# Performance work log

Hardware: AMD Instinct MI355X
Metric: run time of the kernel (lower is better)

Reference implementation:

```python
import jax, jax.numpy as jnp
import numpy as np

L, B, T, TC, T1, D, DK, FF = 4, 4, 1024, 1024, 2048, 384, 256, 1536
TT = 0.1   # lamed blending coefficient (tt in (0,1] path)
EPS = 1e-5


def _ln(x, g, b):
    m = jnp.mean(x, axis=-1, keepdims=True)
    v = jnp.mean((x - m) ** 2, axis=-1, keepdims=True)
    return (x - m) * jax.lax.rsqrt(v + EPS) * g + b


def setup_inputs() -> dict:
    key = jax.random.key(0)
    ks = jax.random.split(key, 16)
    s = 0.02
    return {
        "tgt": jax.random.normal(ks[0], (B, T, D), jnp.float32),
        "memory": jax.random.normal(ks[1], (B, T1, DK), jnp.float32),
        "score_c": jax.random.normal(ks[2], (L, B, TC, T1), jnp.float32),
        "out_c": jax.random.normal(ks[3], (L, B, TC, D), jnp.float32),
        "Wq": jax.random.normal(ks[4], (L, D, D), jnp.float32) * s,
        "bq": jnp.zeros((L, D), jnp.float32),
        "Wk": jax.random.normal(ks[5], (L, D, DK), jnp.float32) * s,
        "bk": jnp.zeros((L, D), jnp.float32),
        "Wv": jax.random.normal(ks[6], (L, D, DK), jnp.float32) * s,
        "bv": jnp.zeros((L, D), jnp.float32),
        "Wkn": jax.random.normal(ks[7], (L, D, D), jnp.float32) * s,
        "bkn": jnp.zeros((L, D), jnp.float32),
        "Wun": jax.random.normal(ks[8], (L, D, D), jnp.float32) * s,
        "bun": jnp.zeros((L, D), jnp.float32),
        "W1": jax.random.normal(ks[9], (L, FF, D), jnp.float32) * s,
        "b1": jnp.zeros((L, FF), jnp.float32),
        "W2": jax.random.normal(ks[10], (L, D, FF), jnp.float32) * s,
        "b2": jnp.zeros((L, D), jnp.float32),
        "g1": jnp.ones((L, D), jnp.float32),
        "be1": jnp.zeros((L, D), jnp.float32),
        "g2": jnp.ones((L, D), jnp.float32),
        "be2": jnp.zeros((L, D), jnp.float32),
    }


def reference(tgt, memory, score_c, out_c, Wq, bq, Wk, bk, Wv, bv,
              Wkn, bkn, Wun, bun, W1, b1, W2, b2, g1, be1, g2, be2):
    scale = 1.0 / np.sqrt(D)
    x = tgt
    for l in range(L):  # fixed small layer count
        # cross-attention q/k/v (n_head = 1)
        q = jnp.einsum('btd,ed->bte', x, Wq[l]) + bq[l]            # [B,T,D]
        k = jnp.einsum('bsk,ek->bse', memory, Wk[l]) + bk[l]       # [B,T1,D]
        v = jnp.einsum('bsk,ek->bse', memory, Wv[l]) + bv[l]       # [B,T1,D]
        att = jnp.einsum('bte,bse->bts', q, k) * scale             # [B,T,T1]
        # blended score path (tt in (0,1])
        unk = jnp.einsum('btd,ed->bte', x, Wun[l]) + bun[l]        # [B,T,D]
        kno = jnp.einsum('bcd,ed->bce', out_c[l], Wkn[l]) + bkn[l] # [B,TC,D]
        score1 = jnp.einsum('bte,bce->btc', unk, kno) * scale      # [B,T,TC]
        mixed = jnp.einsum('btc,bcs->bts', score1, score_c[l])     # [B,T,T1]
        blended = TT * jax.nn.softmax(mixed, axis=-1) \
                  + (1.0 - TT) * jax.nn.softmax(att, axis=-1)
        z = jnp.einsum('bts,bse->bte', blended, v)                 # [B,T,D]
        x = _ln(x + z, g1[l], be1[l])
        h = jax.nn.relu(jnp.einsum('btd,fd->btf', x, W1[l]) + b1[l])
        y2 = jnp.einsum('btf,df->btd', h, W2[l]) + b2[l]
        x = _ln(x + y2, g2[l], be2[l])
    return x
```

## Files before the change

kernel.cpp:

```cpp
#include <hip/hip_runtime.h>
#include <math.h>

#define Lc 4
#define Bc 4
#define Tc 1024
#define TCc 1024
#define T1c 2048
#define Dc 384
#define DKc 256
#define FFc 1536
#define TTc 0.1f
#define EPSc 1e-5f
#define QUc 640

typedef unsigned short u16;
typedef __attribute__((ext_vector_type(8))) __bf16 bf16x8;
typedef __attribute__((ext_vector_type(8))) _Float16 f16x8;
typedef __attribute__((ext_vector_type(4))) float f32x4;

__device__ inline u16 f2bf(float f) {
  union { float f; unsigned u; } x; x.f = f;
  unsigned r = x.u + 0x7fffu + ((x.u >> 16) & 1u);
  return (u16)(r >> 16);
}
__device__ inline float bf2f(u16 v) {
  union { unsigned u; float f; } x; x.u = (unsigned)v << 16; return x.f;
}

struct CDesc { const float* src; u16* dst; long n4; };
struct CPack { CDesc d[16]; long tot4; int nd; };

__global__ void cvt_multi(CPack P) {
  long i = (long)blockIdx.x * 256 + threadIdx.x;
  const long st = (long)gridDim.x * 256;
  for (; i < P.tot4; i += st) {
    long r = i; int g = 0;
    while (g < P.nd - 1 && r >= P.d[g].n4) { r -= P.d[g].n4; ++g; }
    float4 v = ((const float4*)P.d[g].src)[r];
    ushort4 o;
    o.x = f2bf(v.x); o.y = f2bf(v.y); o.z = f2bf(v.z); o.w = f2bf(v.w);
    ((ushort4*)P.d[g].dst)[r] = o;
  }
}

__global__ void make_bias(const float* __restrict__ bq, const float* __restrict__ bun,
                          const u16* __restrict__ wkT, float* __restrict__ bqu) {
  const int l = blockIdx.x, t = threadIdx.x;
  if (t < DKc) {
    const u16* w = wkT + ((long)l * DKc + t) * Dc;
    const float* b = bq + l * Dc;
    float s = 0.f;
    for (int e = 0; e < Dc; ++e) s += b[e] * bf2f(w[e]);
    bqu[l * QUc + t] = s;
  } else {
    bqu[l * QUc + t] = bun[l * Dc + (t - DKc)];
  }
}

__global__ __launch_bounds__(256) void transpose_cvt(const float* __restrict__ src,
                                                     u16* __restrict__ dst,
                                                     int R, int C) {
  __shared__ float t[64 * 65];
  const int z = blockIdx.z;
  const float* s = src + (long)z * R * C;
  u16* d = dst + (long)z * R * C;
  const int s0 = blockIdx.x * 64, c0 = blockIdx.y * 64;
  const int tc = threadIdx.x >> 4;
  const int tx = (threadIdx.x & 15) * 4;
#pragma unroll
  for (int it = 0; it < 4; ++it) {
    const int c = tc + it * 16;
    float4 v = *(const float4*)(s + (long)(c0 + c) * C + s0 + tx);
    float* q = t + c * 65 + tx;
    q[0] = v.x; q[1] = v.y; q[2] = v.z; q[3] = v.w;
  }
  __syncthreads();
#pragma unroll
  for (int it = 0; it < 4; ++it) {
    const int srow = tc + it * 16;
    u16 o[4];
#pragma unroll
    for (int k2 = 0; k2 < 4; ++k2) o[k2] = f2bf(t[(tx + k2) * 65 + srow]);
    *(ushort4*)(d + (long)(s0 + srow) * R + c0 + tx) = *(ushort4*)o;
  }
}

template<int BIAS_MODE, int RELU, int OUT_MODE, int SWIZ, int DUAL>
__global__ __launch_bounds__(256) void gemm_bt(
    const u16* __restrict__ A, const u16* __restrict__ B,
    void* __restrict__ C, const float* __restrict__ bias,
    float alpha, int N, int K, int lda, int ldb,
    long sA, long sB, long sC, long sBias, int ksplit, long sSlab, int bdivA,
    const u16* __restrict__ B2, int ldb2, long sB2, int aoff2,
    void* __restrict__ C2, float alpha2, int nbat, int K2)
{
  __shared__ __attribute__((aligned(16))) u16 As[2][128 * 32];
  __shared__ __attribute__((aligned(16))) u16 Bs[2][128 * 32];
  const int bz = blockIdx.z;
  int b = bz / ksplit;
  const int kc = bz - b * ksplit;
  const u16* Bp = B; int ldbv = ldb; long sBv = sB; void* Cp = C;
  int aoff = 0; float al = alpha; int Kv = K;
  if (DUAL && b >= nbat) {
    b -= nbat; Bp = B2; ldbv = ldb2; sBv = sB2; Cp = C2;
    aoff = aoff2; al = alpha2; Kv = K2;
  }
  const int ba = b / bdivA;
  const int Klen = Kv / ksplit;
  const int k0 = kc * Klen;
  const u16* Ab = A + (long)ba * sA + aoff;
  const u16* Bb = Bp + (long)b * sBv;
  long tm, tn;
  if (SWIZ) {
    const int id = blockIdx.y * 16 + blockIdx.x;
    tm = (long)(id >> 4) * 128;
    tn = (long)(2 * (id & 7) + ((id >> 3) & 1)) * 128;
  } else {
    tm = (long)blockIdx.y * 128; tn = (long)blockIdx.x * 128;
  }
  const int tid = threadIdx.x;
  const int lane = tid & 63, wv = tid >> 6;
  const int wm = (wv >> 1) * 64, wn = (wv & 1) * 64;
  const int q = lane >> 4, r = lane & 15;
  const int ldr = lane >> 2;
  const int ldc = (lane & 3) * 8;

  const u16* gA0 = Ab + (tm + wv * 32 + ldr) * (long)lda + k0 + ldc;
  const u16* gA1 = gA0 + 16 * (long)lda;
  const u16* gB0 = Bb + (tn + wv * 32 + ldr) * (long)ldbv + k0 + ldc;
  const u16* gB1 = gB0 + 16 * (long)ldbv;
  const int dof = (wv * 32 + ldr) * 32 + ldc;

  const f32x4 zero4 = {0.0f, 0.0f, 0.0f, 0.0f};
  f32x4 acc[4][4];
#pragma unroll
  for (int i = 0; i < 4; ++i)
#pragma unroll
    for (int j = 0; j < 4; ++j) acc[i][j] = zero4;

  uint4 ra0 = *(const uint4*)gA0;
  uint4 ra1 = *(const uint4*)gA1;
  uint4 rb0 = *(const uint4*)gB0;
  uint4 rb1 = *(const uint4*)gB1;

  const int iters = Klen >> 5;
  int cur = 0;
  for (int it = 0; it < iters; ++it) {
    u16* a0 = As[cur] + dof;
    u16* b0 = Bs[cur] + dof;
    *(uint4*)a0 = ra0; *(uint4*)(a0 + 512) = ra1;
    *(uint4*)b0 = rb0; *(uint4*)(b0 + 512) = rb1;
    if (it + 1 < iters) {
      const long o = (long)(it + 1) * 32;
      ra0 = *(const uint4*)(gA0 + o);
      ra1 = *(const uint4*)(gA1 + o);
      rb0 = *(const uint4*)(gB0 + o);
      rb1 = *(const uint4*)(gB1 + o);
    }
    __syncthreads();
    bf16x8 af[4], bfr[4];
#pragma unroll
    for (int i = 0; i < 4; ++i) {
      af[i]  = *(const bf16x8*)(As[cur] + (wm + i * 16 + r) * 32 + q * 8);
      bfr[i] = *(const bf16x8*)(Bs[cur] + (wn + i * 16 + r) * 32 + q * 8);
    }
#pragma unroll
    for (int i = 0; i < 4; ++i)
#pragma unroll
      for (int j = 0; j < 4; ++j)
        acc[i][j] = __builtin_amdgcn_mfma_f32_16x16x32_bf16(af[i], bfr[j], acc[i][j], 0, 0, 0);
    cur ^= 1;
  }

  const float* biasb = bias ? bias + (long)ba * sBias : nullptr;
#pragma unroll
  for (int i = 0; i < 4; ++i)
#pragma unroll
    for (int j = 0; j < 4; ++j)
#pragma unroll
      for (int v = 0; v < 4; ++v) {
        long row = tm + wm + i * 16 + q * 4 + v;
        long col = tn + wn + j * 16 + r;
        float val = acc[i][j][v] * al;
        if (BIAS_MODE == 1 && kc == 0) val += biasb[col];
        if (BIAS_MODE == 2 && kc == 0) val += biasb[row];
        if (RELU) val = fmaxf(val, 0.0f);
        long idx = (long)kc * sSlab + (long)b * sC + row * (long)N + col;
        if (OUT_MODE == 0)      ((float*)Cp)[idx] = val;
        else if (OUT_MODE == 1) ((u16*)Cp)[idx] = f2bf(val);
        else                    ((_Float16*)Cp)[idx] = (_Float16)val;
      }
}

__global__ __launch_bounds__(256) void blend_softmax(
    const _Float16* __restrict__ att, const _Float16* __restrict__ mixed,
    u16* __restrict__ out)
{
  const long row = blockIdx.x;
  const int tid = threadIdx.x;
  f16x8 av = *(const f16x8*)(att + row * T1c + tid * 8);
  f16x8 mv = *(const f16x8*)(mixed + row * T1c + tid * 8);
  float a[8], m[8];
#pragma unroll
  for (int i = 0; i < 8; ++i) { a[i] = (float)av[i]; m[i] = (float)mv[i]; }
  float amax = a[0], mmax = m[0];
#pragma unroll
  for (int i = 1; i < 8; ++i) { amax = fmaxf(amax, a[i]); mmax = fmaxf(mmax, m[i]); }
#pragma unroll
  for (int off = 32; off > 0; off >>= 1) {
    amax = fmaxf(amax, __shfl_xor(amax, off));
    mmax = fmaxf(mmax, __shfl_xor(mmax, off));
  }
  __shared__ float red[8];
  const int lane = tid & 63, wv = tid >> 6;
  if (lane == 0) { red[wv] = amax; red[4 + wv] = mmax; }
  __syncthreads();
  amax = fmaxf(fmaxf(red[0], red[1]), fmaxf(red[2], red[3]));
  mmax = fmaxf(fmaxf(red[4], red[5]), fmaxf(red[6], red[7]));
  __syncthreads();
  float asum = 0.f, msum = 0.f;
#pragma unroll
  for (int i = 0; i < 8; ++i) {
    a[i] = __expf(a[i] - amax); asum += a[i];
    m[i] = __expf(m[i] - mmax); msum += m[i];
  }
#pragma unroll
  for (int off = 32; off > 0; off >>= 1) {
    asum += __shfl_xor(asum, off);
    msum += __shfl_xor(msum, off);
  }
  if (lane == 0) { red[wv] = asum; red[4 + wv] = msum; }
  __syncthreads();
  asum = red[0] + red[1] + red[2] + red[3];
  msum = red[4] + red[5] + red[6] + red[7];
  const float ca = (1.0f - TTc) / asum, cm = TTc / msum;
  u16 o[8];
#pragma unroll
  for (int i = 0; i < 8; ++i) o[i] = f2bf(a[i] * ca + m[i] * cm);
  *(uint4*)(out + row * T1c + tid * 8) = *(uint4*)o;
}

__global__ __launch_bounds__(384) void add_ln4(
    const float* __restrict__ xin, const float* __restrict__ zs,
    const float* __restrict__ g, const float* __restrict__ be,
    float* __restrict__ xout, u16* __restrict__ xbf)
{
  const long row = blockIdx.x;
  const int d = threadIdx.x;
  const long SL = (long)Bc * Tc * Dc;
  const long o = row * Dc + d;
  float v = xin[o] + zs[o] + zs[SL + o] + zs[2 * SL + o] + zs[3 * SL + o];
  float s = v, s2 = v * v;
#pragma unroll
  for (int off = 32; off > 0; off >>= 1) {
    s  += __shfl_xor(s, off);
    s2 += __shfl_xor(s2, off);
  }
  __shared__ float red[12];
  const int lane = d & 63, wv = d >> 6;
  if (lane == 0) { red[wv] = s; red[6 + wv] = s2; }
  __syncthreads();
  float S = 0.f, S2 = 0.f;
#pragma unroll
  for (int w = 0; w < 6; ++w) { S += red[w]; S2 += red[6 + w]; }
  const float mean = S * (1.0f / Dc);
  const float var  = S2 * (1.0f / Dc) - mean * mean;
  const float rstd = rsqrtf(var + EPSc);
  const float y = (v - mean) * rstd * g[d] + be[d];
  xout[o] = y;
  xbf[o] = f2bf(y);
}

extern "C" void kernel_launch(void* const* d_in, const int* in_sizes, int n_in,
                              void* d_out, int out_size, void* d_ws, size_t ws_size,
                              hipStream_t stream)
{
  const float* tgt     = (const float*)d_in[0];
  const float* memory  = (const float*)d_in[1];
  const float* score_c = (const float*)d_in[2];
  const float* out_c   = (const float*)d_in[3];
  const float* Wq  = (const float*)d_in[4];  const float* bq  = (const float*)d_in[5];
  const float* Wk  = (const float*)d_in[6];  const float* bk  = (const float*)d_in[7];
  const float* Wv  = (const float*)d_in[8];  const float* bv  = (const float*)d_in[9];
  const float* Wkn = (const float*)d_in[10]; const float* bkn = (const float*)d_in[11];
  const float* Wun = (const float*)d_in[12]; const float* bun = (const float*)d_in[13];
  const float* W1  = (const float*)d_in[14]; const float* b1  = (const float*)d_in[15];
  const float* W2  = (const float*)d_in[16]; const float* b2  = (const float*)d_in[17];
  const float* g1  = (const float*)d_in[18]; const float* be1 = (const float*)d_in[19];
  const float* g2  = (const float*)d_in[20]; const float* be2 = (const float*)d_in[21];
  (void)bk; (void)in_sizes; (void)n_in; (void)out_size;

  char* p = (char*)d_ws;
  auto alloc = [&](size_t b) { char* r = p; p += (b + 255) & ~(size_t)255; return r; };

  u16* wv_bf   = (u16*)alloc((size_t)Lc * Dc * DKc * 2);
  u16* wkn_bf  = (u16*)alloc((size_t)Lc * Dc * Dc * 2);
  u16* w1_bf   = (u16*)alloc((size_t)Lc * FFc * Dc * 2);
  u16* w2_bf   = (u16*)alloc((size_t)Lc * Dc * FFc * 2);
  u16* wqT     = (u16*)alloc((size_t)Lc * Dc * Dc * 2);
  u16* wkT     = (u16*)alloc((size_t)Lc * DKc * Dc * 2);
  u16* wqu_bf  = (u16*)alloc((size_t)Lc * QUc * Dc * 2);
  float* bqu   = (float*)alloc((size_t)Lc * QUc * 4);
  u16* mem_bf  = (u16*)alloc((size_t)Bc * T1c * DKc * 2);
  u16* outc_bf = (u16*)alloc((size_t)Lc * Bc * TCc * Dc * 2);
  u16* x_bf    = (u16*)alloc((size_t)Bc * Tc * Dc * 2);
  float* xbuf  = (float*)alloc((size_t)Bc * Tc * Dc * 4);
  u16* qunk_bf = (u16*)alloc((size_t)Bc * Tc * QUc * 2);
  u16* vT_all  = (u16*)alloc((size_t)Bc * Lc * Dc * T1c * 2);
  u16* knoT_all = (u16*)alloc((size_t)Lc * Bc * Dc * TCc * 2);
  u16* M2T_all = (u16*)alloc((size_t)Lc * Bc * T1c * Dc * 2);
  u16* scT_all = (u16*)alloc((size_t)Lc * Bc * T1c * TCc * 2);
  _Float16* att   = (_Float16*)alloc((size_t)Bc * Tc * T1c * 2);
  _Float16* mixed = (_Float16*)alloc((size_t)Bc * Tc * T1c * 2);
  u16* blended = (u16*)alloc((size_t)Bc * Tc * T1c * 2);
  float* zslab = (float*)alloc((size_t)4 * Bc * Tc * Dc * 4);
  float* yslab = (float*)alloc((size_t)4 * Bc * Tc * Dc * 4);
  u16* h_bf    = (u16*)alloc((size_t)Bc * Tc * FFc * 2);

  if ((size_t)(p - (char*)d_ws) > ws_size) return;

  {
    CPack cp{}; int g = 0; long tot4 = 0;
    auto add = [&](const float* s, u16* d, long n) {
      cp.d[g].src = s; cp.d[g].dst = d; cp.d[g].n4 = n / 4; tot4 += n / 4; ++g;
    };
    add(Wv,  wv_bf,  (long)Lc * Dc * DKc);
    add(Wkn, wkn_bf, (long)Lc * Dc * Dc);
    add(W1,  w1_bf,  (long)Lc * FFc * Dc);
    add(W2,  w2_bf,  (long)Lc * Dc * FFc);
    add(memory, mem_bf, (long)Bc * T1c * DKc);
    add(out_c, outc_bf, (long)Lc * Bc * TCc * Dc);
    add(tgt, x_bf, (long)Bc * Tc * Dc);
    for (int l = 0; l < Lc; ++l)
      add(Wun + (long)l * Dc * Dc,
          wqu_bf + (long)l * QUc * Dc + (long)DKc * Dc, (long)Dc * Dc);
    cp.nd = g; cp.tot4 = tot4;
    cvt_multi<<<4096, 256, 0, stream>>>(cp);
  }

  transpose_cvt<<<dim3(T1c / 64, TCc / 64, Lc * Bc), 256, 0, stream>>>(
      score_c, scT_all, TCc, T1c);
  transpose_cvt<<<dim3(Dc / 64, Dc / 64, Lc), 256, 0, stream>>>(Wq, wqT, Dc, Dc);
  transpose_cvt<<<dim3(DKc / 64, Dc / 64, Lc), 256, 0, stream>>>(Wk, wkT, Dc, DKc);

  const float scale = 1.0f / sqrtf((float)Dc);
  const long SLAB = (long)Bc * Tc * Dc;

  gemm_bt<0,0,1,0,0><<<dim3(Dc/128, DKc/128, Lc), 256, 0, stream>>>(
      wkT, wqT, wqu_bf, nullptr, 1.0f, Dc, Dc, Dc, Dc,
      (long)DKc*Dc, (long)Dc*Dc, (long)QUc*Dc, 0, 1, 0, 1,
      nullptr, 0, 0, 0, nullptr, 0.f, 0, Dc);
  make_bias<<<Lc, QUc, 0, stream>>>(bq, bun, wkT, bqu);

  gemm_bt<2,0,1,0,0><<<dim3(T1c/128, Lc*Dc/128, Bc), 256, 0, stream>>>(
      wv_bf, mem_bf, vT_all, bv, 1.0f, T1c, DKc, DKc, DKc,
      0, (long)T1c*DKc, (long)Lc*Dc*T1c, 0, 1, 0, 1,
      nullptr, 0, 0, 0, nullptr, 0.f, 0, DKc);
  gemm_bt<2,0,1,0,0><<<dim3(TCc/128, Dc/128, Lc*Bc), 256, 0, stream>>>(
      wkn_bf, outc_bf, knoT_all, bkn, 1.0f, TCc, Dc, Dc, Dc,
      (long)Dc*Dc, (long)TCc*Dc, (long)Dc*TCc, Dc, 1, 0, Bc,
      nullptr, 0, 0, 0, nullptr, 0.f, 0, Dc);
  gemm_bt<0,0,1,0,0><<<dim3(Dc/128, T1c/128, Lc*Bc), 256, 0, stream>>>(
      scT_all, knoT_all, M2T_all, nullptr, scale, Dc, TCc, TCc, TCc,
      (long)T1c*TCc, (long)Dc*TCc, (long)T1c*Dc, 0, 1, 0, 1,
      nullptr, 0, 0, 0, nullptr, 0.f, 0, TCc);

  for (int l = 0; l < Lc; ++l) {
    gemm_bt<1,0,1,0,0><<<dim3(QUc/128, Bc*Tc/128, 1), 256, 0, stream>>>(
        x_bf, wqu_bf + (long)l*QUc*Dc, qunk_bf, bqu + l*QUc,
        1.0f, QUc, Dc, Dc, Dc, 0, 0, 0, 0, 1, 0, 1,
        nullptr, 0, 0, 0, nullptr, 0.f, 0, Dc);
    gemm_bt<0,0,2,1,1><<<dim3(T1c/128, Tc/128, 2*Bc), 256, 0, stream>>>(
        qunk_bf, mem_bf, att, nullptr, scale, T1c, DKc, QUc, DKc,
        (long)Tc*QUc, (long)T1c*DKc, (long)Tc*T1c, 0, 1, 0, 1,
        M2T_all + (long)l*Bc*T1c*Dc, Dc, (long)T1c*Dc, DKc, mixed, 1.0f, Bc, Dc);
    blend_softmax<<<Bc*Tc, 256, 0, stream>>>(att, mixed, blended);
    gemm_bt<0,0,0,0,0><<<dim3(Dc/128, Tc/128, Bc*4), 256, 0, stream>>>(
        blended, vT_all + (long)l*Dc*T1c, zslab, nullptr, 1.0f,
        Dc, T1c, T1c, T1c, (long)Tc*T1c, (long)Lc*Dc*T1c, (long)Tc*Dc, 0, 4, SLAB, 1,
        nullptr, 0, 0, 0, nullptr, 0.f, 0, T1c);
    add_ln4<<<Bc*Tc, Dc, 0, stream>>>(
        (l == 0) ? tgt : xbuf, zslab, g1 + l*Dc, be1 + l*Dc, xbuf, x_bf);
    gemm_bt<1,1,1,0,0><<<dim3(FFc/128, Bc*Tc/128, 1), 256, 0, stream>>>(
        x_bf, w1_bf + (long)l*FFc*Dc, h_bf, b1 + l*FFc, 1.0f,
        FFc, Dc, Dc, Dc, 0, 0, 0, 0, 1, 0, 1,
        nullptr, 0, 0, 0, nullptr, 0.f, 0, Dc);
    gemm_bt<1,0,0,0,0><<<dim3(Dc/128, Bc*Tc/128, 4), 256, 0, stream>>>(
        h_bf, w2_bf + (long)l*Dc*FFc, yslab, b2 + l*Dc, 1.0f,
        Dc, FFc, FFc, FFc, 0, 0, 0, 0, 4, SLAB, 1,
        nullptr, 0, 0, 0, nullptr, 0.f, 0, FFc);
    add_ln4<<<Bc*Tc, Dc, 0, stream>>>(
        xbuf, yslab, g2 + l*Dc, be2 + l*Dc,
        (l == Lc - 1) ? (float*)d_out : xbuf, x_bf);
  }
}
```

Before: 939.2 us.

## Fuse blended softmax into attention-V GEMM A-load and read out_c as fp32

Replaces the blend_softmax kernel with a per-row stats kernel that writes only max and scale for both softmaxes. The z GEMM's A-operand load then reads the fp16 att and mixed tiles and rebuilds the blended bf16 probabilities on the fly. This removes the write and reread of the blended matrix. Separately, the kno GEMM now reads out_c directly as fp32 and converts it to bf16 while staging into shared memory, dropping that slice of the conversion pass. The cost is that every N-tile of the z GEMM reads twice the A data and recomputes the exponentials redundantly.

```diff
diff --git a/kernel.cpp b/kernel.cpp
--- a/kernel.cpp
+++ b/kernel.cpp
@@ -85,14 +85,15 @@
   }
 }
 
-template<int BIAS_MODE, int RELU, int OUT_MODE, int SWIZ, int DUAL>
+template<int BIAS_MODE, int RELU, int OUT_MODE, int SWIZ, int DUAL, int FUSEA, int BF32>
 __global__ __launch_bounds__(256) void gemm_bt(
     const u16* __restrict__ A, const u16* __restrict__ B,
     void* __restrict__ C, const float* __restrict__ bias,
     float alpha, int N, int K, int lda, int ldb,
     long sA, long sB, long sC, long sBias, int ksplit, long sSlab, int bdivA,
     const u16* __restrict__ B2, int ldb2, long sB2, int aoff2,
-    void* __restrict__ C2, float alpha2, int nbat, int K2)
+    void* __restrict__ C2, float alpha2, int nbat, int K2,
+    const u16* __restrict__ Am, const float* __restrict__ st4)
 {
   __shared__ __attribute__((aligned(16))) u16 As[2][128 * 32];
   __shared__ __attribute__((aligned(16))) u16 Bs[2][128 * 32];
@@ -138,24 +139,78 @@
 #pragma unroll
     for (int j = 0; j < 4; ++j) acc[i][j] = zero4;
 
-  uint4 ra0 = *(const uint4*)gA0;
-  uint4 ra1 = *(const uint4*)gA1;
-  uint4 rb0 = *(const uint4*)gB0;
-  uint4 rb1 = *(const uint4*)gB1;
+  uint4 ra0, ra1, rb0, rb1;
+  f16x8 av0, av1, mv0, mv1;
+  float4 qb0a, qb0b, qb1a, qb1b;
+  const u16* gM0 = nullptr; const u16* gM1 = nullptr;
+  const float* fB0 = nullptr; const float* fB1 = nullptr;
+  float4 st0, st1;
+  if (FUSEA) {
+    gM0 = Am + (gA0 - A);
+    gM1 = Am + (gA1 - A);
+    av0 = *(const f16x8*)gA0; mv0 = *(const f16x8*)gM0;
+    av1 = *(const f16x8*)gA1; mv1 = *(const f16x8*)gM1;
+    const long r0 = (long)b * Tc + tm + wv * 32 + ldr;
+    st0 = ((const float4*)st4)[r0];
+    st1 = ((const float4*)st4)[r0 + 16];
+  } else {
+    ra0 = *(const uint4*)gA0; ra1 = *(const uint4*)gA1;
+  }
+  if (BF32) {
+    const float* Bf = (const float*)B + (long)b * sBv;
+    fB0 = Bf + (tn + wv * 32 + ldr) * (long)ldbv + k0 + ldc;
+    fB1 = fB0 + 16 * (long)ldbv;
+    qb0a = *(const float4*)fB0; qb0b = *(const float4*)(fB0 + 4);
+    qb1a = *(const float4*)fB1; qb1b = *(const float4*)(fB1 + 4);
+  } else {
+    rb0 = *(const uint4*)gB0; rb1 = *(const uint4*)gB1;
+  }
 
   const int iters = Klen >> 5;
   int cur = 0;
   for (int it = 0; it < iters; ++it) {
     u16* a0 = As[cur] + dof;
     u16* b0 = Bs[cur] + dof;
-    *(uint4*)a0 = ra0; *(uint4*)(a0 + 512) = ra1;
-    *(uint4*)b0 = rb0; *(uint4*)(b0 + 512) = rb1;
+    if (FUSEA) {
+      u16 oa[16];
+#pragma unroll
+      for (int e2 = 0; e2 < 8; ++e2) {
+        oa[e2]     = f2bf(__expf((float)av0[e2] - st0.x) * st0.y
+                        + __expf((float)mv0[e2] - st0.z) * st0.w);
+        oa[8 + e2] = f2bf(__expf((float)av1[e2] - st1.x) * st1.y
+                        + __expf((float)mv1[e2] - st1.z) * st1.w);
+      }
+      *(uint4*)a0 = ((uint4*)oa)[0]; *(uint4*)(a0 + 512) = ((uint4*)oa)[1];
+    } else {
+      *(uint4*)a0 = ra0; *(uint4*)(a0 + 512) = ra1;
+    }
+    if (BF32) {
+      u16 ob[16];
+#pragma unroll
+      for (int e2 = 0; e2 < 4; ++e2) {
+        ob[e2]      = f2bf(((const float*)&qb0a)[e2]);
+        ob[4 + e2]  = f2bf(((const float*)&qb0b)[e2]);
+        ob[8 + e2]  = f2bf(((const float*)&qb1a)[e2]);
+        ob[12 + e2] = f2bf(((const float*)&qb1b)[e2]);
+      }
+      *(uint4*)b0 = ((uint4*)ob)[0]; *(uint4*)(b0 + 512) = ((uint4*)ob)[1];
+    } else {
+      *(uint4*)b0 = rb0; *(uint4*)(b0 + 512) = rb1;
+    }
     if (it + 1 < iters) {
       const long o = (long)(it + 1) * 32;
-      ra0 = *(const uint4*)(gA0 + o);
-      ra1 = *(const uint4*)(gA1 + o);
-      rb0 = *(const uint4*)(gB0 + o);
-      rb1 = *(const uint4*)(gB1 + o);
+      if (FUSEA) {
+        av0 = *(const f16x8*)(gA0 + o); mv0 = *(const f16x8*)(gM0 + o);
+        av1 = *(const f16x8*)(gA1 + o); mv1 = *(const f16x8*)(gM1 + o);
+      } else {
+        ra0 = *(const uint4*)(gA0 + o); ra1 = *(const uint4*)(gA1 + o);
+      }
+      if (BF32) {
+        qb0a = *(const float4*)(fB0 + o); qb0b = *(const float4*)(fB0 + o + 4);
+        qb1a = *(const float4*)(fB1 + o); qb1b = *(const float4*)(fB1 + o + 4);
+      } else {
+        rb0 = *(const uint4*)(gB0 + o); rb1 = *(const uint4*)(gB1 + o);
+      }
     }
     __syncthreads();
     bf16x8 af[4], bfr[4];
@@ -192,9 +247,9 @@
       }
 }
 
-__global__ __launch_bounds__(256) void blend_softmax(
+__global__ __launch_bounds__(256) void blend_stats(
     const _Float16* __restrict__ att, const _Float16* __restrict__ mixed,
-    u16* __restrict__ out)
+    float4* __restrict__ st)
 {
   const long row = blockIdx.x;
   const int tid = threadIdx.x;
@@ -221,8 +276,8 @@
   float asum = 0.f, msum = 0.f;
 #pragma unroll
   for (int i = 0; i < 8; ++i) {
-    a[i] = __expf(a[i] - amax); asum += a[i];
-    m[i] = __expf(m[i] - mmax); msum += m[i];
+    asum += __expf(a[i] - amax);
+    msum += __expf(m[i] - mmax);
   }
 #pragma unroll
   for (int off = 32; off > 0; off >>= 1) {
@@ -233,11 +288,12 @@
   __syncthreads();
   asum = red[0] + red[1] + red[2] + red[3];
   msum = red[4] + red[5] + red[6] + red[7];
-  const float ca = (1.0f - TTc) / asum, cm = TTc / msum;
-  u16 o[8];
-#pragma unroll
-  for (int i = 0; i < 8; ++i) o[i] = f2bf(a[i] * ca + m[i] * cm);
-  *(uint4*)(out + row * T1c + tid * 8) = *(uint4*)o;
+  if (tid == 0) {
+    float4 o;
+    o.x = amax; o.y = (1.0f - TTc) / asum;
+    o.z = mmax; o.w = TTc / msum;
+    st[row] = o;
+  }
 }
 
 __global__ __launch_bounds__(384) void add_ln4(
@@ -302,7 +358,6 @@
   u16* wqu_bf  = (u16*)alloc((size_t)Lc * QUc * Dc * 2);
   float* bqu   = (float*)alloc((size_t)Lc * QUc * 4);
   u16* mem_bf  = (u16*)alloc((size_t)Bc * T1c * DKc * 2);
-  u16* outc_bf = (u16*)alloc((size_t)Lc * Bc * TCc * Dc * 2);
   u16* x_bf    = (u16*)alloc((size_t)Bc * Tc * Dc * 2);
   float* xbuf  = (float*)alloc((size_t)Bc * Tc * Dc * 4);
   u16* qunk_bf = (u16*)alloc((size_t)Bc * Tc * QUc * 2);
@@ -312,7 +367,7 @@
   u16* scT_all = (u16*)alloc((size_t)Lc * Bc * T1c * TCc * 2);
   _Float16* att   = (_Float16*)alloc((size_t)Bc * Tc * T1c * 2);
   _Float16* mixed = (_Float16*)alloc((size_t)Bc * Tc * T1c * 2);
-  u16* blended = (u16*)alloc((size_t)Bc * Tc * T1c * 2);
+  float4* stats = (float4*)alloc((size_t)Bc * Tc * 16);
   float* zslab = (float*)alloc((size_t)4 * Bc * Tc * Dc * 4);
   float* yslab = (float*)alloc((size_t)4 * Bc * Tc * Dc * 4);
   u16* h_bf    = (u16*)alloc((size_t)Bc * Tc * FFc * 2);
@@ -329,7 +384,6 @@
     add(W1,  w1_bf,  (long)Lc * FFc * Dc);
     add(W2,  w2_bf,  (long)Lc * Dc * FFc);
     add(memory, mem_bf, (long)Bc * T1c * DKc);
-    add(out_c, outc_bf, (long)Lc * Bc * TCc * Dc);
     add(tgt, x_bf, (long)Bc * Tc * Dc);
     for (int l = 0; l < Lc; ++l)
       add(Wun + (long)l * Dc * Dc,
@@ -346,49 +400,51 @@
   const float scale = 1.0f / sqrtf((float)Dc);
   const long SLAB = (long)Bc * Tc * Dc;
 
-  gemm_bt<0,0,1,0,0><<<dim3(Dc/128, DKc/128, Lc), 256, 0, stream>>>(
+  gemm_bt<0,0,1,0,0,0,0><<<dim3(Dc/128, DKc/128, Lc), 256, 0, stream>>>(
       wkT, wqT, wqu_bf, nullptr, 1.0f, Dc, Dc, Dc, Dc,
       (long)DKc*Dc, (long)Dc*Dc, (long)QUc*Dc, 0, 1, 0, 1,
-      nullptr, 0, 0, 0, nullptr, 0.f, 0, Dc);
+      nullptr, 0, 0, 0, nullptr, 0.f, 0, Dc, nullptr, nullptr);
   make_bias<<<Lc, QUc, 0, stream>>>(bq, bun, wkT, bqu);
 
-  gemm_bt<2,0,1,0,0><<<dim3(T1c/128, Lc*Dc/128, Bc), 256, 0, stream>>>(
+  gemm_bt<2,0,1,0,0,0,0><<<dim3(T1c/128, Lc*Dc/128, Bc), 256, 0, stream>>>(
       wv_bf, mem_bf, vT_all, bv, 1.0f, T1c, DKc, DKc, DKc,
       0, (long)T1c*DKc, (long)Lc*Dc*T1c, 0, 1, 0, 1,
-      nullptr, 0, 0, 0, nullptr, 0.f, 0, DKc);
-  gemm_bt<2,0,1,0,0><<<dim3(TCc/128, Dc/128, Lc*Bc), 256, 0, stream>>>(
-      wkn_bf, outc_bf, knoT_all, bkn, 1.0f, TCc, Dc, Dc, Dc,
+      nullptr, 0, 0, 0, nullptr, 0.f, 0, DKc, nullptr, nullptr);
+  gemm_bt<2,0,1,0,0,0,1><<<dim3(TCc/128, Dc/128, Lc*Bc), 256, 0, stream>>>(
+      wkn_bf, (const u16*)out_c, knoT_all, bkn, 1.0f, TCc, Dc, Dc, Dc,
       (long)Dc*Dc, (long)TCc*Dc, (long)Dc*TCc, Dc, 1, 0, Bc,
-      nullptr, 0, 0, 0, nullptr, 0.f, 0, Dc);
-  gemm_bt<0,0,1,0,0><<<dim3(Dc/128, T1c/128, Lc*Bc), 256, 0, stream>>>(
+      nullptr, 0, 0, 0, nullptr, 0.f, 0, Dc, nullptr, nullptr);
+  gemm_bt<0,0,1,0,0,0,0><<<dim3(Dc/128, T1c/128, Lc*Bc), 256, 0, stream>>>(
       scT_all, knoT_all, M2T_all, nullptr, scale, Dc, TCc, TCc, TCc,
       (long)T1c*TCc, (long)Dc*TCc, (long)T1c*Dc, 0, 1, 0, 1,
-      nullptr, 0, 0, 0, nullptr, 0.f, 0, TCc);
+      nullptr, 0, 0, 0, nullptr, 0.f, 0, TCc, nullptr, nullptr);
 
   for (int l = 0; l < Lc; ++l) {
-    gemm_bt<1,0,1,0,0><<<dim3(QUc/128, Bc*Tc/128, 1), 256, 0, stream>>>(
+    gemm_bt<1,0,1,0,0,0,0><<<dim3(QUc/128, Bc*Tc/128, 1), 256, 0, stream>>>(
         x_bf, wqu_bf + (long)l*QUc*Dc, qunk_bf, bqu + l*QUc,
         1.0f, QUc, Dc, Dc, Dc, 0, 0, 0, 0, 1, 0, 1,
-        nullptr, 0, 0, 0, nullptr, 0.f, 0, Dc);
-    gemm_bt<0,0,2,1,1><<<dim3(T1c/128, Tc/128, 2*Bc), 256, 0, stream>>>(
+        nullptr, 0, 0, 0, nullptr, 0.f, 0, Dc, nullptr, nullptr);
+    gemm_bt<0,0,2,1,1,0,0><<<dim3(T1c/128, Tc/128, 2*Bc), 256, 0, stream>>>(
         qunk_bf, mem_bf, att, nullptr, scale, T1c, DKc, QUc, DKc,
         (long)Tc*QUc, (long)T1c*DKc, (long)Tc*T1c, 0, 1, 0, 1,
-        M2T_all + (long)l*Bc*T1c*Dc, Dc, (long)T1c*Dc, DKc, mixed, 1.0f, Bc, Dc);
-    blend_softmax<<<Bc*Tc, 256, 0, stream>>>(att, mixed, blended);
-    gemm_bt<0,0,0,0,0><<<dim3(Dc/128, Tc/128, Bc*4), 256, 0, stream>>>(
-        blended, vT_all + (long)l*Dc*T1c, zslab, nullptr, 1.0f,
+        M2T_all + (long)l*Bc*T1c*Dc, Dc, (long)T1c*Dc, DKc, mixed, 1.0f, Bc, Dc,
+        nullptr, nullptr);
+    blend_stats<<<Bc*Tc, 256, 0, stream>>>(att, mixed, stats);
+    gemm_bt<0,0,0,0,0,1,0><<<dim3(Dc/128, Tc/128, Bc*4), 256, 0, stream>>>(
+        (const u16*)att, vT_all + (long)l*Dc*T1c, zslab, nullptr, 1.0f,
         Dc, T1c, T1c, T1c, (long)Tc*T1c, (long)Lc*Dc*T1c, (long)Tc*Dc, 0, 4, SLAB, 1,
-        nullptr, 0, 0, 0, nullptr, 0.f, 0, T1c);
+        nullptr, 0, 0, 0, nullptr, 0.f, 0, T1c,
+        (const u16*)mixed, (const float*)stats);
     add_ln4<<<Bc*Tc, Dc, 0, stream>>>(
         (l == 0) ? tgt : xbuf, zslab, g1 + l*Dc, be1 + l*Dc, xbuf, x_bf);
-    gemm_bt<1,1,1,0,0><<<dim3(FFc/128, Bc*Tc/128, 1), 256, 0, stream>>>(
+    gemm_bt<1,1,1,0,0,0,0><<<dim3(FFc/128, Bc*Tc/128, 1), 256, 0, stream>>>(
         x_bf, w1_bf + (long)l*FFc*Dc, h_bf, b1 + l*FFc, 1.0f,
         FFc, Dc, Dc, Dc, 0, 0, 0, 0, 1, 0, 1,
-        nullptr, 0, 0, 0, nullptr, 0.f, 0, Dc);
-    gemm_bt<1,0,0,0,0><<<dim3(Dc/128, Bc*Tc/128, 4), 256, 0, stream>>>(
+        nullptr, 0, 0, 0, nullptr, 0.f, 0, Dc, nullptr, nullptr);
+    gemm_bt<1,0,0,0,0,0,0><<<dim3(Dc/128, Bc*Tc/128, 4), 256, 0, stream>>>(
         h_bf, w2_bf + (long)l*Dc*FFc, yslab, b2 + l*Dc, 1.0f,
         Dc, FFc, FFc, FFc, 0, 0, 0, 0, 4, SLAB, 1,
-        nullptr, 0, 0, 0, nullptr, 0.f, 0, FFc);
+        nullptr, 0, 0, 0, nullptr, 0.f, 0, FFc, nullptr, nullptr);
     add_ln4<<<Bc*Tc, Dc, 0, stream>>>(
         xbuf, yslab, g2 + l*Dc, be2 + l*Dc,
         (l == Lc - 1) ? (float*)d_out : xbuf, x_bf);
```

New measurement: 973.4 us. 3.6% more time.
